# Optimization experiments

Hardware: AMD Instinct MI355X
Metric: run time of the kernel (lower is better)

## Reference

```python
import jax, jax.numpy as jnp
import numpy as np

H = 256
EPS = 1e-5
WIN = (-2, -1, 1, 2)  # radius_graph(pos/2^(d+1), k=2) on unit-spaced timestamps


def leaky(x):
    return jnp.where(x >= 0, x, 0.2 * x)


def layernorm(x, g, b):
    mu = jnp.mean(x, axis=-1, keepdims=True)
    var = jnp.mean(jnp.square(x - mu), axis=-1, keepdims=True)
    return (x - mu) * jax.lax.rsqrt(var + EPS) * g + b


def nbr_mean(x, offsets):
    # mean over temporal-window neighbors within each video row; [B,T,C]
    if not offsets:
        return jnp.zeros_like(x)
    T = x.shape[1]
    idx = jnp.arange(T)
    acc = jnp.zeros_like(x)
    cnt = jnp.zeros((T,), x.dtype)
    for o in offsets:
        valid = (idx + o >= 0) & (idx + o < T)
        acc = acc + jnp.where(valid[None, :, None], jnp.roll(x, -o, axis=1), 0.0)
        cnt = cnt + valid.astype(x.dtype)
    return acc / jnp.maximum(cnt, 1.0)[None, :, None]


def conv(x, Ws, Wn, b, offsets):
    # GraphConv with mean aggregation: W_self x_i + W_nbr mean_j x_j + b
    return x @ Ws + nbr_mean(x, offsets) @ Wn + b


def stage(x, s, Wself, Wnbr, bconv, ln_g, ln_b, offsets):
    # Dropout(eval)=id; conv; LeakyReLU(0.2); conv; LayerNorm; LeakyReLU(0.2)
    x = leaky(conv(x, Wself[s, 0], Wnbr[s, 0], bconv[s, 0], offsets))
    x = conv(x, Wself[s, 1], Wnbr[s, 1], bconv[s, 1], offsets)
    return leaky(layernorm(x, ln_g[s], ln_b[s]))


def upsample2(c):
    # knn_interpolate(k=2) from coarse (stride-2 subsampled) grid back to fine grid:
    # even fine nodes coincide with a coarse node (dist 0 -> weight ~inf -> copy);
    # odd fine nodes are equidistant from two coarse nodes (0.5/0.5), except the
    # last odd node whose 2-NN are at dist s and 3s -> weights 0.9/0.1.
    even = c
    nxt = jnp.concatenate([c[:, 1:], c[:, -1:]], axis=1)
    odd = 0.5 * (c + nxt)
    odd = odd.at[:, -1].set(0.9 * c[:, -1] + 0.1 * c[:, -2])
    B, Tc, C = c.shape
    return jnp.stack([even, odd], axis=2).reshape(B, 2 * Tc, C)


def setup_inputs() -> dict:
    key = jax.random.key(0)
    ks = jax.random.split(key, 8)
    B, T, F = 16, 4096, 1024
    N = B * T
    x = jax.random.normal(ks[0], (N, 1, F), dtype=jnp.float32)
    pos = (jnp.arange(N) % T).astype(jnp.float32)
    batch = (jnp.arange(N) // T).astype(jnp.int64)
    indices = (jnp.arange(N) % T).astype(jnp.int64)
    Wp = jax.random.normal(ks[1], (F, H), dtype=jnp.float32) / np.sqrt(F)
    bp = jnp.zeros((H,), jnp.float32)
    Wself = jax.random.normal(ks[2], (6, 2, H, H), dtype=jnp.float32) / np.sqrt(H)
    Wnbr = jax.random.normal(ks[3], (6, 2, H, H), dtype=jnp.float32) / np.sqrt(H)
    bconv = jnp.zeros((6, 2, H), jnp.float32)
    ln_g = jnp.ones((6, H), jnp.float32)
    ln_b = jnp.zeros((6, H), jnp.float32)
    return {"x": x, "pos": pos, "batch": batch, "indices": indices, "B": B, "T": T,
            "Wp": Wp, "bp": bp, "Wself": Wself, "Wnbr": Wnbr, "bconv": bconv,
            "ln_g": ln_g, "ln_b": ln_b}


def reference(x, pos, batch, indices, B, T, Wp, bp, Wself, Wnbr, bconv, ln_g, ln_b):
    # input projection: Rearrange 'B S F -> B (S F)' (S=1) + Linear
    feat = x.reshape(B, T, -1) @ Wp + bp  # [B,T,H]
    # ---- Temporal Encoder ----
    f = feat
    skips = [feat]  # depth-0 input graph features
    for d in range(3):
        f = f[:, ::2]  # batch_subsampling time pooling (stride 2)
        f = f + stage(f, d, Wself, Wnbr, bconv, ln_g, ln_b, WIN)
        if d < 2:
            skips.append(f)
    # ---- Function-Aware Decoder (eval path: clustering_at_inference=False) ----
    for i in range(3):
        res = skips[2 - i]
        f = res + upsample2(f)  # knn_interpolate(k=2) + skip
        dep = 2 - i
        # radius_graph(indices, 1.5): pooled index spacing 2^dep > 1.5 for dep>=1 -> no edges
        offs = WIN if dep == 0 else ()
        f = stage(f, 3 + i, Wself, Wnbr, bconv, ln_g, ln_b, offs)
    return f  # finest-resolution decoder output [B,T,H]
```

## Files before the change

### kernel.cpp

```cpp
#include <hip/hip_runtime.h>

#define HH 256

typedef __attribute__((ext_vector_type(8))) short short8;
typedef __attribute__((ext_vector_type(4))) float f32x4;
typedef __attribute__((ext_vector_type(4))) unsigned short u16x4;
typedef __attribute__((ext_vector_type(8))) unsigned short u16x8;

constexpr int NBATCH = 16;
constexpr int T0   = 4096;
constexpr int FDIM = 1024;
constexpr int R0   = NBATCH * T0;
constexpr int R1   = R0 / 2;
constexpr int R2   = R0 / 4;
constexpr int R3   = R0 / 8;

__device__ __forceinline__ float b2f(unsigned short u) {
    union { unsigned int i; float f; } v; v.i = ((unsigned int)u) << 16; return v.f;
}
__device__ __forceinline__ unsigned short f2b(float f) {
    union { float f; unsigned int i; } v; v.f = f;
    unsigned int r = v.i + 0x7fffu + ((v.i >> 16) & 1u);
    return (unsigned short)(r >> 16);
}
__device__ __forceinline__ void gload16(const void* g, void* l) {
    __builtin_amdgcn_global_load_lds((const __attribute__((address_space(1))) void*)g,
                                     (__attribute__((address_space(3))) void*)l, 16, 0, 0);
}
__device__ __forceinline__ void barrier_sync() {
    asm volatile("s_waitcnt lgkmcnt(0)\n\ts_barrier" ::: "memory");
}
__device__ __forceinline__ void wait_vm(int n) {
    switch (n) {
    case 2:  asm volatile("s_waitcnt vmcnt(2)"  ::: "memory"); break;
    case 3:  asm volatile("s_waitcnt vmcnt(3)"  ::: "memory"); break;
    case 4:  asm volatile("s_waitcnt vmcnt(4)"  ::: "memory"); break;
    case 5:  asm volatile("s_waitcnt vmcnt(5)"  ::: "memory"); break;
    case 6:  asm volatile("s_waitcnt vmcnt(6)"  ::: "memory"); break;
    default: asm volatile("s_waitcnt vmcnt(0)"  ::: "memory"); break;
    }
}
__device__ __forceinline__ int swz_ks(int chunk)        { return (chunk & 3) ^ ((chunk >> 3) & 3); }
__device__ __forceinline__ int frag_idx(int row, int g) { return (row * 4 + (g ^ ((row >> 1) & 3))) * 8; }

struct PVv { u16x8 v0, v1, v2, v3; };

__device__ __forceinline__ void transpose_tile(const float* __restrict__ src,
                                               unsigned short* __restrict__ dst,
                                               int K, int tilesPerMat, int bid, int tidx)
{
    int m = bid / tilesPerMat;
    int t = bid % tilesPerMat;
    int tr = t >> 3, tc = t & 7;
    const float* S = src + (size_t)m * K * HH;
    unsigned short* D = dst + (size_t)m * HH * K;
    __shared__ float tile[32][33];
    int x = tidx & 31, y = tidx >> 5;
#pragma unroll
    for (int i = y; i < 32; i += 8)
        tile[i][x] = S[(size_t)(tr * 32 + i) * HH + tc * 32 + x];
    __syncthreads();
#pragma unroll
    for (int i = y; i < 32; i += 8)
        D[(size_t)(tc * 32 + i) * K + tr * 32 + x] = f2b(tile[x][i]);
}

__global__ void transpose_all(const float* __restrict__ Wself, const float* __restrict__ Wnbr,
                              const float* __restrict__ Wp,
                              unsigned short* __restrict__ Ws_t, unsigned short* __restrict__ Wn_t,
                              unsigned short* __restrict__ Wp_t)
{
    int bid = blockIdx.x;
    if (bid < 768)       transpose_tile(Wself, Ws_t, HH,   64,  bid,        threadIdx.x);
    else if (bid < 1536) transpose_tile(Wnbr,  Wn_t, HH,   64,  bid - 768,  threadIdx.x);
    else                 transpose_tile(Wp,    Wp_t, FDIM, 256, bid - 1536, threadIdx.x);
}

template<int BM, int AMODE, int NBR, int LNFUSE, int OUT>
__launch_bounds__(512)
__global__ void conv_fused(const unsigned short* __restrict__ A,
                           const unsigned short* __restrict__ Cc,
                           const unsigned short* __restrict__ prev,
                           const unsigned short* __restrict__ Bself,
                           const unsigned short* __restrict__ Bnbr,
                           const float* __restrict__ bias,
                           const float* __restrict__ lng,
                           const float* __restrict__ lnb,
                           void* __restrict__ dstv,
                           int Tl, int Tc, int tlshift)
{
    constexpr int NT = NBR ? 16 : 8;
    constexpr int MF = (BM + 31) / 32;
    constexpr int WROWS = BM / 2;
    __shared__ unsigned short As[3][BM * 32];
    __shared__ unsigned short Bs[3][256 * 32];
    __shared__ float lnred[LNFUSE ? BM : 1][8];

    const int tid  = threadIdx.x;
    const int lane = tid & 63;
    const int w    = tid >> 6;
    const int wm   = w & 1, wn = w >> 1;
    const long row0 = (long)blockIdx.x * BM;

    const bool hasA   = (tid < BM * 4);
    const bool hasA_w = (w < (BM * 4) / 64);
    const int arr = tid >> 2;
    const int akk = swz_ks(tid);
    const long gr = row0 + (hasA ? arr : 0);

    float ca = 0.f, cb = 0.f; size_t rc0 = 0, rc1 = 0;
    if (AMODE == 2) {
        int t = (int)(gr & (long)(Tl - 1));
        long bq = gr >> tlshift;
        int k = t >> 1;
        rc0 = (size_t)bq * Tc + k;
        if (!(t & 1))        { ca = 1.0f; cb = 0.0f; rc1 = rc0; }
        else if (k < Tc - 1) { ca = 0.5f; cb = 0.5f; rc1 = rc0 + 1; }
        else                 { ca = 0.9f; cb = 0.1f; rc1 = rc0 - 1; }
    }
    float vinv = 1.f;
    float cf0 = 0.f, cf1 = 0.f, cf2 = 0.f, cf3 = 0.f;
    size_t nrow0 = 0, nrow1 = 0, nrow2 = 0, nrow3 = 0;
    if (NBR) {
        const int offs[4] = {-2, -1, 1, 2};
        int t = (int)(gr & (long)(Tl - 1));
        int cnt = 0;
        float cf[4]; size_t nr[4];
#pragma unroll
        for (int oi = 0; oi < 4; oi++) {
            int tn = t + offs[oi];
            bool v = (tn >= 0 && tn < Tl);
            cnt += v ? 1 : 0;
            int tcl = tn < 0 ? 0 : (tn > Tl - 1 ? Tl - 1 : tn);
            long r = gr - t + tcl;
            nr[oi] = (size_t)((AMODE == 1) ? 2 * r : r) * HH;
            cf[oi] = v ? 1.f : 0.f;
        }
        vinv = 1.f / (float)cnt;
        cf0 = cf[0]; cf1 = cf[1]; cf2 = cf[2]; cf3 = cf[3];
        nrow0 = nr[0]; nrow1 = nr[1]; nrow2 = nr[2]; nrow3 = nr[3];
    }

    f32x4 acc[MF][4] = {};
    PVv pvE = {}, pvO = {};

    auto Lof = [&](int t) -> int {
        if (!hasA_w) return 2;
        const int seg = (NBR && t >= 8) ? 1 : 0;
        return seg ? 6 : (AMODE == 2 ? 5 : 3);
    };
    auto issueB = [&](int t) {
        const int seg = (NBR && t >= 8) ? 1 : 0;
        const int k0 = (t & 7) * 32;
        const int sl = t % 3;
        const unsigned short* __restrict__ Bm = seg ? Bnbr : Bself;
        gload16(Bm + (size_t)arr * HH + k0 + akk * 8,         &Bs[sl][tid * 8]);
        gload16(Bm + (size_t)(128 + arr) * HH + k0 + akk * 8, &Bs[sl][(tid + 512) * 8]);
    };
    auto issueA = [&](int t, PVv& pv) {
        if (!hasA) return;
        const int seg = (NBR && t >= 8) ? 1 : 0;
        const int k0 = (t & 7) * 32;
        const int sl = t % 3;
        if (seg == 0) {
            if (AMODE == 0) {
                gload16(A + (size_t)gr * HH + k0 + akk * 8, &As[sl][tid * 8]);
            } else if (AMODE == 1) {
                gload16(A + (size_t)(2 * gr) * HH + k0 + akk * 8, &As[sl][tid * 8]);
            } else {
                pv.v0 = *(const u16x8*)(A + (size_t)gr * HH + k0 + akk * 8);
                pv.v1 = *(const u16x8*)(Cc + rc0 * HH + k0 + akk * 8);
                pv.v2 = *(const u16x8*)(Cc + rc1 * HH + k0 + akk * 8);
            }
        } else {
            pv.v0 = *(const u16x8*)(A + nrow0 + k0 + akk * 8);
            pv.v1 = *(const u16x8*)(A + nrow1 + k0 + akk * 8);
            pv.v2 = *(const u16x8*)(A + nrow2 + k0 + akk * 8);
            pv.v3 = *(const u16x8*)(A + nrow3 + k0 + akk * 8);
        }
    };
    auto finishA = [&](int t, PVv& pv) {
        if (!hasA) return;
        const int seg = (NBR && t >= 8) ? 1 : 0;
        const int sl = t % 3;
        if (seg == 0) {
            if (AMODE == 2) {
                u16x8 o;
#pragma unroll
                for (int j = 0; j < 8; j++)
                    o[j] = f2b(b2f(pv.v0[j]) + ca * b2f(pv.v1[j]) + cb * b2f(pv.v2[j]));
                *(u16x8*)&As[sl][tid * 8] = o;
            }
        } else {
            u16x8 o;
#pragma unroll
            for (int j = 0; j < 8; j++) {
                float a = cf0 * b2f(pv.v0[j]) + cf1 * b2f(pv.v1[j])
                        + cf2 * b2f(pv.v2[j]) + cf3 * b2f(pv.v3[j]);
                o[j] = f2b(a * vinv);
            }
            *(u16x8*)&As[sl][tid * 8] = o;
        }
    };

    issueB(0); issueA(0, pvE);
    issueB(1); issueA(1, pvO);
    wait_vm(Lof(1));
    finishA(0, pvE);
    barrier_sync();

#pragma unroll
    for (int t = 0; t < NT; ++t) {
        if (t + 2 < NT) {
            issueB(t + 2);
            if (((t + 2) & 1) == 0) issueA(t + 2, pvE); else issueA(t + 2, pvO);
        }

        const int sl = t % 3;
        __builtin_amdgcn_s_setprio(1);
        short8 af[MF], bg[4];
#pragma unroll
        for (int i = 0; i < MF; i++)
            af[i] = *(const short8*)&As[sl][frag_idx(wm * WROWS + i * 16 + (lane & 15), lane >> 4)];
#pragma unroll
        for (int i = 0; i < 4; i++)
            bg[i] = *(const short8*)&Bs[sl][frag_idx(wn * 64 + i * 16 + (lane & 15), lane >> 4)];
#pragma unroll
        for (int mi = 0; mi < MF; mi++)
#pragma unroll
            for (int ni = 0; ni < 4; ni++)
                acc[mi][ni] = __builtin_amdgcn_mfma_f32_16x16x32_bf16(af[mi], bg[ni], acc[mi][ni], 0, 0, 0);
        __builtin_amdgcn_s_setprio(0);

        if (t + 1 < NT) {
            wait_vm((t + 2 < NT) ? Lof(t + 2) : 0);
            if (((t + 1) & 1) == 0) finishA(t + 1, pvE); else finishA(t + 1, pvO);
            barrier_sync();
        }
    }

    if (LNFUSE == 0) {
        unsigned short* outp = (unsigned short*)dstv;
#pragma unroll
        for (int mi = 0; mi < MF; mi++) {
            size_t rbase = (size_t)row0 + wm * WROWS + mi * 16 + (lane >> 4) * 4;
#pragma unroll
            for (int ni = 0; ni < 4; ni++) {
                int c = wn * 64 + ni * 16 + (lane & 15);
                float bb = bias[c];
                f32x4 v = acc[mi][ni];
#pragma unroll
                for (int r = 0; r < 4; r++) {
                    float t = v[r] + bb;
                    t = (t >= 0.f) ? t : 0.2f * t;
                    outp[(rbase + r) * HH + c] = f2b(t);
                }
            }
        }
    } else {
        float bb[4];
#pragma unroll
        for (int ni = 0; ni < 4; ni++) bb[ni] = bias[wn * 64 + ni * 16 + (lane & 15)];

#pragma unroll
        for (int mi = 0; mi < MF; mi++) {
#pragma unroll
            for (int r = 0; r < 4; r++) {
                float s = 0.f, q = 0.f;
#pragma unroll
                for (int ni = 0; ni < 4; ni++) {
                    float v = acc[mi][ni][r] + bb[ni];
                    s += v; q += v * v;
                }
                s += __shfl_xor(s, 1); q += __shfl_xor(q, 1);
                s += __shfl_xor(s, 2); q += __shfl_xor(q, 2);
                s += __shfl_xor(s, 4); q += __shfl_xor(q, 4);
                s += __shfl_xor(s, 8); q += __shfl_xor(q, 8);
                if ((lane & 15) == 0) {
                    int row = wm * WROWS + mi * 16 + (lane >> 4) * 4 + r;
                    lnred[row][wn]     = s;
                    lnred[row][4 + wn] = q;
                }
            }
        }
        __syncthreads();

        float gv[4], bv[4];
#pragma unroll
        for (int ni = 0; ni < 4; ni++) {
            int c = wn * 64 + ni * 16 + (lane & 15);
            gv[ni] = lng[c]; bv[ni] = lnb[c];
        }

#pragma unroll
        for (int mi = 0; mi < MF; mi++) {
#pragma unroll
            for (int r = 0; r < 4; r++) {
                int row = wm * WROWS + mi * 16 + (lane >> 4) * 4 + r;
                float s = lnred[row][0] + lnred[row][1] + lnred[row][2] + lnred[row][3];
                float q = lnred[row][4] + lnred[row][5] + lnred[row][6] + lnred[row][7];
                float mu  = s * (1.0f / HH);
                float var = q * (1.0f / HH) - mu * mu;
                float inv = rsqrtf(var + 1e-5f);
                size_t grow = (size_t)row0 + row;
#pragma unroll
                for (int ni = 0; ni < 4; ni++) {
                    int c = wn * 64 + ni * 16 + (lane & 15);
                    float v = acc[mi][ni][r] + bb[ni];
                    float y = (v - mu) * inv * gv[ni] + bv[ni];
                    y = (y >= 0.f) ? y : 0.2f * y;
                    if (OUT == 2) {
                        ((float*)dstv)[grow * HH + c] = y;
                    } else {
                        if (OUT == 1) y += b2f(prev[(2 * grow) * HH + c]);
                        ((unsigned short*)dstv)[grow * HH + c] = f2b(y);
                    }
                }
            }
        }
    }
}

__launch_bounds__(512)
__global__ void proj_gemm(const float* __restrict__ A, const unsigned short* __restrict__ Bt,
                          const float* __restrict__ bias, unsigned short* __restrict__ out)
{
    constexpr int NT = FDIM / 32;
    __shared__ unsigned short As[3][128 * 32];
    __shared__ unsigned short Bs[3][256 * 32];
    const int tid  = threadIdx.x;
    const int lane = tid & 63;
    const int w    = tid >> 6;
    const int wm   = w & 1, wn = w >> 1;
    const size_t row0 = (size_t)blockIdx.x * 128;

    const int arr = tid >> 2;
    const int akk = swz_ks(tid);

    f32x4 acc[4][4] = {};
    float4 paE0, paE1, paO0, paO1;

    auto issue = [&](int t, float4& p0, float4& p1) {
        const int k0 = t * 32;
        const int sl = t % 3;
        gload16(Bt + (size_t)arr * FDIM + k0 + akk * 8,         &Bs[sl][tid * 8]);
        gload16(Bt + (size_t)(128 + arr) * FDIM + k0 + akk * 8, &Bs[sl][(tid + 512) * 8]);
        const float* s = A + (row0 + arr) * (size_t)FDIM + k0 + akk * 8;
        p0 = *(const float4*)s;
        p1 = *(const float4*)(s + 4);
    };
    auto finish = [&](int t, float4& p0, float4& p1) {
        const int sl = t % 3;
        u16x8 o = { f2b(p0.x), f2b(p0.y), f2b(p0.z), f2b(p0.w),
                    f2b(p1.x), f2b(p1.y), f2b(p1.z), f2b(p1.w) };
        *(u16x8*)&As[sl][tid * 8] = o;
    };

    issue(0, paE0, paE1);
    issue(1, paO0, paO1);
    wait_vm(4);
    finish(0, paE0, paE1);
    barrier_sync();

#pragma unroll
    for (int t = 0; t < NT; ++t) {
        if (t + 2 < NT) {
            if (((t + 2) & 1) == 0) issue(t + 2, paE0, paE1); else issue(t + 2, paO0, paO1);
        }

        const int sl = t % 3;
        __builtin_amdgcn_s_setprio(1);
        short8 af[4], bg[4];
#pragma unroll
        for (int i = 0; i < 4; i++) {
            af[i] = *(const short8*)&As[sl][frag_idx(wm * 64 + i * 16 + (lane & 15), lane >> 4)];
            bg[i] = *(const short8*)&Bs[sl][frag_idx(wn * 64 + i * 16 + (lane & 15), lane >> 4)];
        }
#pragma unroll
        for (int mi = 0; mi < 4; mi++)
#pragma unroll
            for (int ni = 0; ni < 4; ni++)
                acc[mi][ni] = __builtin_amdgcn_mfma_f32_16x16x32_bf16(af[mi], bg[ni], acc[mi][ni], 0, 0, 0);
        __builtin_amdgcn_s_setprio(0);

        if (t + 1 < NT) {
            wait_vm((t + 2 < NT) ? 4 : 0);
            if (((t + 1) & 1) == 0) finish(t + 1, paE0, paE1); else finish(t + 1, paO0, paO1);
            barrier_sync();
        }
    }

#pragma unroll
    for (int mi = 0; mi < 4; mi++) {
        size_t rbase = row0 + wm * 64 + mi * 16 + (lane >> 4) * 4;
#pragma unroll
        for (int ni = 0; ni < 4; ni++) {
            int c = wn * 64 + ni * 16 + (lane & 15);
            float bb = bias[c];
            f32x4 v = acc[mi][ni];
#pragma unroll
            for (int r = 0; r < 4; r++)
                out[(rbase + r) * HH + c] = f2b(v[r] + bb);
        }
    }
}

__global__ void upsample_add_kernel(unsigned short* __restrict__ res, const unsigned short* __restrict__ c,
                                    int Tc, int tlshift, int Rout)
{
    int idx = blockIdx.x * 256 + threadIdx.x;
    int r = idx >> 5, cc = (idx & 31) * 8;
    if (r >= Rout) return;
    int Tl = Tc * 2;
    int t  = r & (Tl - 1);
    int bq = r >> tlshift;
    int k  = t >> 1;
    size_t rc = (size_t)bq * Tc + k;
    float u[8];
    if (!(t & 1)) {
        u16x8 v = *(const u16x8*)(c + rc * HH + cc);
#pragma unroll
        for (int j = 0; j < 8; j++) u[j] = b2f(v[j]);
    } else if (k < Tc - 1) {
        u16x8 v0 = *(const u16x8*)(c + rc * HH + cc);
        u16x8 v1 = *(const u16x8*)(c + (rc + 1) * HH + cc);
#pragma unroll
        for (int j = 0; j < 8; j++) u[j] = 0.5f * (b2f(v0[j]) + b2f(v1[j]));
    } else {
        u16x8 v0 = *(const u16x8*)(c + rc * HH + cc);
        u16x8 vm = *(const u16x8*)(c + (rc - 1) * HH + cc);
#pragma unroll
        for (int j = 0; j < 8; j++) u[j] = 0.9f * b2f(v0[j]) + 0.1f * b2f(vm[j]);
    }
    u16x8 rv = *(const u16x8*)(res + (size_t)r * HH + cc);
    u16x8 o;
#pragma unroll
    for (int j = 0; j < 8; j++) o[j] = f2b(b2f(rv[j]) + u[j]);
    *(u16x8*)(res + (size_t)r * HH + cc) = o;
}

extern "C" void kernel_launch(void* const* d_in, const int* in_sizes, int n_in,
                              void* d_out, int out_size, void* d_ws, size_t ws_size,
                              hipStream_t stream)
{
    const float* x     = (const float*)d_in[0];
    const float* Wp    = (const float*)d_in[6];
    const float* bp    = (const float*)d_in[7];
    const float* Wself = (const float*)d_in[8];
    const float* Wnbr  = (const float*)d_in[9];
    const float* bconv = (const float*)d_in[10];
    const float* ln_g  = (const float*)d_in[11];
    const float* ln_b  = (const float*)d_in[12];
    float* out = (float*)d_out;

    char* p = (char*)d_ws;
    unsigned short* Wself_t = (unsigned short*)p; p += (size_t)12 * HH * HH * 2;
    unsigned short* Wnbr_t  = (unsigned short*)p; p += (size_t)12 * HH * HH * 2;
    unsigned short* Wp_t    = (unsigned short*)p; p += (size_t)HH * FDIM * 2;
    unsigned short* c0 = (unsigned short*)p; p += (size_t)R0 * HH * 2;
    unsigned short* c1 = (unsigned short*)p; p += (size_t)R1 * HH * 2;
    unsigned short* c2 = (unsigned short*)p; p += (size_t)R2 * HH * 2;
    unsigned short* c3 = (unsigned short*)p; p += (size_t)R3 * HH * 2;
    unsigned short* t1 = (unsigned short*)p; p += (size_t)R0 * HH * 2;
    if (ws_size < (size_t)(p - (char*)d_ws)) return;

    auto Ws = [&](int i) { return Wself_t + (size_t)i * HH * HH; };
    auto Wn = [&](int i) { return Wnbr_t  + (size_t)i * HH * HH; };

    transpose_all<<<1792, 256, 0, stream>>>(Wself, Wnbr, Wp, Wself_t, Wnbr_t, Wp_t);

    proj_gemm<<<R0 / 128, 512, 0, stream>>>(x, Wp_t, bp, c0);

    conv_fused<128, 1, 1, 0, 0><<<R1 / 128, 512, 0, stream>>>(c0, nullptr, nullptr, Ws(0), Wn(0),
        bconv + 0 * HH, nullptr, nullptr, t1, 2048, 0, 0);
    conv_fused<128, 0, 1, 1, 1><<<R1 / 128, 512, 0, stream>>>(t1, nullptr, c0, Ws(1), Wn(1),
        bconv + 1 * HH, ln_g + 0 * HH, ln_b + 0 * HH, c1, 2048, 0, 0);

    conv_fused<64, 1, 1, 0, 0><<<R2 / 64, 512, 0, stream>>>(c1, nullptr, nullptr, Ws(2), Wn(2),
        bconv + 2 * HH, nullptr, nullptr, t1, 1024, 0, 0);
    conv_fused<64, 0, 1, 1, 1><<<R2 / 64, 512, 0, stream>>>(t1, nullptr, c1, Ws(3), Wn(3),
        bconv + 3 * HH, ln_g + 1 * HH, ln_b + 1 * HH, c2, 1024, 0, 0);

    conv_fused<32, 1, 1, 0, 0><<<R3 / 32, 512, 0, stream>>>(c2, nullptr, nullptr, Ws(4), Wn(4),
        bconv + 4 * HH, nullptr, nullptr, t1, 512, 0, 0);
    conv_fused<32, 0, 1, 1, 1><<<R3 / 32, 512, 0, stream>>>(t1, nullptr, c2, Ws(5), Wn(5),
        bconv + 5 * HH, ln_g + 2 * HH, ln_b + 2 * HH, c3, 512, 0, 0);

    conv_fused<64, 2, 0, 0, 0><<<R2 / 64, 512, 0, stream>>>(c2, c3, nullptr, Ws(6), nullptr,
        bconv + 6 * HH, nullptr, nullptr, t1, 1024, 512, 10);
    conv_fused<64, 0, 0, 1, 0><<<R2 / 64, 512, 0, stream>>>(t1, nullptr, nullptr, Ws(7), nullptr,
        bconv + 7 * HH, ln_g + 3 * HH, ln_b + 3 * HH, c2, 1024, 0, 0);

    conv_fused<128, 2, 0, 0, 0><<<R1 / 128, 512, 0, stream>>>(c1, c2, nullptr, Ws(8), nullptr,
        bconv + 8 * HH, nullptr, nullptr, t1, 2048, 1024, 11);
    conv_fused<128, 0, 0, 1, 0><<<R1 / 128, 512, 0, stream>>>(t1, nullptr, nullptr, Ws(9), nullptr,
        bconv + 9 * HH, ln_g + 4 * HH, ln_b + 4 * HH, c1, 2048, 0, 0);

    upsample_add_kernel<<<R0 / 8, 256, 0, stream>>>(c0, c1, 2048, 12, R0);
    conv_fused<128, 0, 1, 0, 0><<<R0 / 128, 512, 0, stream>>>(c0, nullptr, nullptr, Ws(10), Wn(10),
        bconv + 10 * HH, nullptr, nullptr, t1, 4096, 0, 0);
    conv_fused<128, 0, 1, 1, 2><<<R0 / 128, 512, 0, stream>>>(t1, nullptr, nullptr, Ws(11), Wn(11),
        bconv + 11 * HH, ln_g + 5 * HH, ln_b + 5 * HH, out, 4096, 0, 0);
}
```

Measured before the change: 353.1 us.

## Single-buffer register-staged A loads and raise occupancy via launch bounds

Replaces the even/odd double set of register-staged A-tile prefetch buffers with a single buffer. The register-path load for tile t+2 is now issued after tile t+1 is finished into shared memory, and the vmcnt wait counts shrink to match. Both GEMM kernels also declare launch_bounds(512,4) to cap registers and allow more resident waves. The cost is a shorter prefetch distance for register-staged loads, which exposes more global latency, and possible spills under the tighter register cap.

Result: slower. 411.4 us (+16.5%).

```diff
diff --git a/kernel.cpp b/kernel.cpp
--- a/kernel.cpp
+++ b/kernel.cpp
@@ -77,7 +77,7 @@
 }
 
 template<int BM, int AMODE, int NBR, int LNFUSE, int OUT>
-__launch_bounds__(512)
+__launch_bounds__(512, 4)
 __global__ void conv_fused(const unsigned short* __restrict__ A,
                            const unsigned short* __restrict__ Cc,
                            const unsigned short* __restrict__ prev,
@@ -142,32 +142,33 @@
     }
 
     f32x4 acc[MF][4] = {};
-    PVv pvE = {}, pvO = {};
-
-    auto Lof = [&](int t) -> int {
+    PVv pv = {};
+
+    auto NG = [&](int t) -> int {
         if (!hasA_w) return 2;
         const int seg = (NBR && t >= 8) ? 1 : 0;
-        return seg ? 6 : (AMODE == 2 ? 5 : 3);
-    };
-    auto issueB = [&](int t) {
+        return (seg == 0 && AMODE <= 1) ? 3 : 2;
+    };
+    auto issueG = [&](int t) {
         const int seg = (NBR && t >= 8) ? 1 : 0;
         const int k0 = (t & 7) * 32;
         const int sl = t % 3;
         const unsigned short* __restrict__ Bm = seg ? Bnbr : Bself;
         gload16(Bm + (size_t)arr * HH + k0 + akk * 8,         &Bs[sl][tid * 8]);
         gload16(Bm + (size_t)(128 + arr) * HH + k0 + akk * 8, &Bs[sl][(tid + 512) * 8]);
-    };
-    auto issueA = [&](int t, PVv& pv) {
+        if (hasA && seg == 0 && AMODE <= 1) {
+            if (AMODE == 0)
+                gload16(A + (size_t)gr * HH + k0 + akk * 8, &As[sl][tid * 8]);
+            else
+                gload16(A + (size_t)(2 * gr) * HH + k0 + akk * 8, &As[sl][tid * 8]);
+        }
+    };
+    auto issueR = [&](int t) {
         if (!hasA) return;
         const int seg = (NBR && t >= 8) ? 1 : 0;
         const int k0 = (t & 7) * 32;
-        const int sl = t % 3;
         if (seg == 0) {
-            if (AMODE == 0) {
-                gload16(A + (size_t)gr * HH + k0 + akk * 8, &As[sl][tid * 8]);
-            } else if (AMODE == 1) {
-                gload16(A + (size_t)(2 * gr) * HH + k0 + akk * 8, &As[sl][tid * 8]);
-            } else {
+            if (AMODE == 2) {
                 pv.v0 = *(const u16x8*)(A + (size_t)gr * HH + k0 + akk * 8);
                 pv.v1 = *(const u16x8*)(Cc + rc0 * HH + k0 + akk * 8);
                 pv.v2 = *(const u16x8*)(Cc + rc1 * HH + k0 + akk * 8);
@@ -179,7 +180,7 @@
             pv.v3 = *(const u16x8*)(A + nrow3 + k0 + akk * 8);
         }
     };
-    auto finishA = [&](int t, PVv& pv) {
+    auto finishA = [&](int t) {
         if (!hasA) return;
         const int seg = (NBR && t >= 8) ? 1 : 0;
         const int sl = t % 3;
@@ -203,18 +204,17 @@
         }
     };
 
-    issueB(0); issueA(0, pvE);
-    issueB(1); issueA(1, pvO);
-    wait_vm(Lof(1));
-    finishA(0, pvE);
+    issueG(0);
+    issueR(0);
+    issueG(1);
+    wait_vm(NG(1));
+    finishA(0);
+    issueR(1);
     barrier_sync();
 
 #pragma unroll
     for (int t = 0; t < NT; ++t) {
-        if (t + 2 < NT) {
-            issueB(t + 2);
-            if (((t + 2) & 1) == 0) issueA(t + 2, pvE); else issueA(t + 2, pvO);
-        }
+        if (t + 2 < NT) issueG(t + 2);
 
         const int sl = t % 3;
         __builtin_amdgcn_s_setprio(1);
@@ -233,8 +233,9 @@
         __builtin_amdgcn_s_setprio(0);
 
         if (t + 1 < NT) {
-            wait_vm((t + 2 < NT) ? Lof(t + 2) : 0);
-            if (((t + 1) & 1) == 0) finishA(t + 1, pvE); else finishA(t + 1, pvO);
+            wait_vm((t + 2 < NT) ? NG(t + 2) : 0);
+            finishA(t + 1);
+            if (t + 2 < NT) issueR(t + 2);
             barrier_sync();
         }
     }
@@ -321,7 +322,7 @@
     }
 }
 
-__launch_bounds__(512)
+__launch_bounds__(512, 4)
 __global__ void proj_gemm(const float* __restrict__ A, const unsigned short* __restrict__ Bt,
                           const float* __restrict__ bias, unsigned short* __restrict__ out)
 {
@@ -338,35 +339,38 @@
     const int akk = swz_ks(tid);
 
     f32x4 acc[4][4] = {};
-    float4 paE0, paE1, paO0, paO1;
-
-    auto issue = [&](int t, float4& p0, float4& p1) {
+    float4 pa0, pa1;
+
+    auto issueG = [&](int t) {
         const int k0 = t * 32;
         const int sl = t % 3;
         gload16(Bt + (size_t)arr * FDIM + k0 + akk * 8,         &Bs[sl][tid * 8]);
         gload16(Bt + (size_t)(128 + arr) * FDIM + k0 + akk * 8, &Bs[sl][(tid + 512) * 8]);
+    };
+    auto issueR = [&](int t) {
+        const int k0 = t * 32;
         const float* s = A + (row0 + arr) * (size_t)FDIM + k0 + akk * 8;
-        p0 = *(const float4*)s;
-        p1 = *(const float4*)(s + 4);
-    };
-    auto finish = [&](int t, float4& p0, float4& p1) {
+        pa0 = *(const float4*)s;
+        pa1 = *(const float4*)(s + 4);
+    };
+    auto finish = [&](int t) {
         const int sl = t % 3;
-        u16x8 o = { f2b(p0.x), f2b(p0.y), f2b(p0.z), f2b(p0.w),
-                    f2b(p1.x), f2b(p1.y), f2b(p1.z), f2b(p1.w) };
+        u16x8 o = { f2b(pa0.x), f2b(pa0.y), f2b(pa0.z), f2b(pa0.w),
+                    f2b(pa1.x), f2b(pa1.y), f2b(pa1.z), f2b(pa1.w) };
         *(u16x8*)&As[sl][tid * 8] = o;
     };
 
-    issue(0, paE0, paE1);
-    issue(1, paO0, paO1);
-    wait_vm(4);
-    finish(0, paE0, paE1);
+    issueG(0);
+    issueR(0);
+    issueG(1);
+    wait_vm(2);
+    finish(0);
+    issueR(1);
     barrier_sync();
 
 #pragma unroll
     for (int t = 0; t < NT; ++t) {
-        if (t + 2 < NT) {
-            if (((t + 2) & 1) == 0) issue(t + 2, paE0, paE1); else issue(t + 2, paO0, paO1);
-        }
+        if (t + 2 < NT) issueG(t + 2);
 
         const int sl = t % 3;
         __builtin_amdgcn_s_setprio(1);
@@ -384,8 +388,9 @@
         __builtin_amdgcn_s_setprio(0);
 
         if (t + 1 < NT) {
-            wait_vm((t + 2 < NT) ? 4 : 0);
-            if (((t + 1) & 1) == 0) finish(t + 1, paE0, paE1); else finish(t + 1, paO0, paO1);
+            wait_vm((t + 2 < NT) ? 2 : 0);
+            finish(t + 1);
+            if (t + 2 < NT) issueR(t + 2);
             barrier_sync();
         }
     }
```

## Fuse both decoder-stage convs into one kernel keeping intermediate in LDS

Applied to the files above, without the earlier changes.

Adds up_stage_fused, which performs the upsample+skip add, the first self-only conv with LeakyReLU, stores the intermediate activations in shared memory, then runs the second conv with LayerNorm and LeakyReLU in the same kernel. This replaces two kernel launches per decoder stage for depths 2 and 1, and removes the global write and re-read of the intermediate tensor. The cost is a larger LDS footprint (an extra BM×256 bf16 buffer), which may reduce occupancy. The depth-1 stage also moves from 128-row to 64-row tiles. The output is written in place over the skip input, which appears safe because each block reads only its own rows of that buffer.

After: 350.1 us (median of 2 runs). About the same (-0.8%).

```diff
diff --git a/kernel.cpp b/kernel.cpp
--- a/kernel.cpp
+++ b/kernel.cpp
@@ -42,6 +42,7 @@
 }
 __device__ __forceinline__ int swz_ks(int chunk)        { return (chunk & 3) ^ ((chunk >> 3) & 3); }
 __device__ __forceinline__ int frag_idx(int row, int g) { return (row * 4 + (g ^ ((row >> 1) & 3))) * 8; }
+__device__ __forceinline__ int a2_idx(int row, int g)   { return (row * 32 + (g ^ (row & 31))) * 8; }
 
 struct PVv { u16x8 v0, v1, v2, v3; };
 
@@ -321,6 +322,231 @@
     }
 }
 
+template<int BM>
+__launch_bounds__(512)
+__global__ void up_stage_fused(const unsigned short* __restrict__ A,
+                               const unsigned short* __restrict__ Cc,
+                               const unsigned short* __restrict__ B1,
+                               const float* __restrict__ b1,
+                               const unsigned short* __restrict__ B2,
+                               const float* __restrict__ b2,
+                               const float* __restrict__ lng,
+                               const float* __restrict__ lnb,
+                               unsigned short* __restrict__ dst,
+                               int Tl, int Tc, int tlshift)
+{
+    constexpr int MF = BM / 32;
+    constexpr int WROWS = BM / 2;
+    __shared__ unsigned short As[3][BM * 32];
+    __shared__ unsigned short Bs[3][256 * 32];
+    __shared__ unsigned short A2[BM * 256];
+    __shared__ float lnred[BM][8];
+
+    const int tid  = threadIdx.x;
+    const int lane = tid & 63;
+    const int w    = tid >> 6;
+    const int wm   = w & 1, wn = w >> 1;
+    const long row0 = (long)blockIdx.x * BM;
+
+    const bool hasA   = (tid < BM * 4);
+    const bool hasA_w = (w < (BM * 4) / 64);
+    const int arr = tid >> 2;
+    const int akk = swz_ks(tid);
+    const long gr = row0 + (hasA ? arr : 0);
+
+    float ca, cb; size_t rc0, rc1;
+    {
+        int t = (int)(gr & (long)(Tl - 1));
+        long bq = gr >> tlshift;
+        int k = t >> 1;
+        rc0 = (size_t)bq * Tc + k;
+        if (!(t & 1))        { ca = 1.0f; cb = 0.0f; rc1 = rc0; }
+        else if (k < Tc - 1) { ca = 0.5f; cb = 0.5f; rc1 = rc0 + 1; }
+        else                 { ca = 0.9f; cb = 0.1f; rc1 = rc0 - 1; }
+    }
+
+    f32x4 acc[MF][4] = {};
+    PVv pvE = {}, pvO = {};
+
+    auto issueB1 = [&](int t) {
+        const int k0 = t * 32;
+        const int sl = t % 3;
+        gload16(B1 + (size_t)arr * HH + k0 + akk * 8,         &Bs[sl][tid * 8]);
+        gload16(B1 + (size_t)(128 + arr) * HH + k0 + akk * 8, &Bs[sl][(tid + 512) * 8]);
+    };
+    auto issueA1 = [&](int t, PVv& pv) {
+        if (!hasA) return;
+        const int k0 = t * 32;
+        pv.v0 = *(const u16x8*)(A + (size_t)gr * HH + k0 + akk * 8);
+        pv.v1 = *(const u16x8*)(Cc + rc0 * HH + k0 + akk * 8);
+        pv.v2 = *(const u16x8*)(Cc + rc1 * HH + k0 + akk * 8);
+    };
+    auto finishA1 = [&](int t, PVv& pv) {
+        if (!hasA) return;
+        const int sl = t % 3;
+        u16x8 o;
+#pragma unroll
+        for (int j = 0; j < 8; j++)
+            o[j] = f2b(b2f(pv.v0[j]) + ca * b2f(pv.v1[j]) + cb * b2f(pv.v2[j]));
+        *(u16x8*)&As[sl][tid * 8] = o;
+    };
+    const int L1 = hasA_w ? 5 : 2;
+
+    issueB1(0); issueA1(0, pvE);
+    issueB1(1); issueA1(1, pvO);
+    wait_vm(L1);
+    finishA1(0, pvE);
+    barrier_sync();
+
+#pragma unroll
+    for (int t = 0; t < 8; ++t) {
+        if (t + 2 < 8) {
+            issueB1(t + 2);
+            if (((t + 2) & 1) == 0) issueA1(t + 2, pvE); else issueA1(t + 2, pvO);
+        }
+        const int sl = t % 3;
+        __builtin_amdgcn_s_setprio(1);
+        short8 af[MF], bg[4];
+#pragma unroll
+        for (int i = 0; i < MF; i++)
+            af[i] = *(const short8*)&As[sl][frag_idx(wm * WROWS + i * 16 + (lane & 15), lane >> 4)];
+#pragma unroll
+        for (int i = 0; i < 4; i++)
+            bg[i] = *(const short8*)&Bs[sl][frag_idx(wn * 64 + i * 16 + (lane & 15), lane >> 4)];
+#pragma unroll
+        for (int mi = 0; mi < MF; mi++)
+#pragma unroll
+            for (int ni = 0; ni < 4; ni++)
+                acc[mi][ni] = __builtin_amdgcn_mfma_f32_16x16x32_bf16(af[mi], bg[ni], acc[mi][ni], 0, 0, 0);
+        __builtin_amdgcn_s_setprio(0);
+        if (t + 1 < 8) {
+            wait_vm((t + 2 < 8) ? L1 : 0);
+            if (((t + 1) & 1) == 0) finishA1(t + 1, pvE); else finishA1(t + 1, pvO);
+            barrier_sync();
+        }
+    }
+
+#pragma unroll
+    for (int mi = 0; mi < MF; mi++) {
+#pragma unroll
+        for (int ni = 0; ni < 4; ni++) {
+            int c = wn * 64 + ni * 16 + (lane & 15);
+            float bb1 = b1[c];
+            int g = c >> 3, e = c & 7;
+            f32x4 v = acc[mi][ni];
+#pragma unroll
+            for (int r = 0; r < 4; r++) {
+                int row = wm * WROWS + mi * 16 + (lane >> 4) * 4 + r;
+                float t = v[r] + bb1;
+                t = (t >= 0.f) ? t : 0.2f * t;
+                A2[a2_idx(row, g) + e] = f2b(t);
+            }
+        }
+    }
+    __syncthreads();
+
+#pragma unroll
+    for (int mi = 0; mi < MF; mi++)
+#pragma unroll
+        for (int ni = 0; ni < 4; ni++)
+            acc[mi][ni] = f32x4{};
+
+    auto issueB2 = [&](int t) {
+        const int k0 = t * 32;
+        const int sl = t % 3;
+        gload16(B2 + (size_t)arr * HH + k0 + akk * 8,         &Bs[sl][tid * 8]);
+        gload16(B2 + (size_t)(128 + arr) * HH + k0 + akk * 8, &Bs[sl][(tid + 512) * 8]);
+    };
+
+    issueB2(0);
+    issueB2(1);
+    wait_vm(2);
+    barrier_sync();
+
+#pragma unroll
+    for (int t = 0; t < 8; ++t) {
+        if (t + 2 < 8) issueB2(t + 2);
+        const int sl = t % 3;
+        __builtin_amdgcn_s_setprio(1);
+        short8 af[MF], bg[4];
+#pragma unroll
+        for (int i = 0; i < MF; i++) {
+            int row = wm * WROWS + i * 16 + (lane & 15);
+            int g = t * 4 + (lane >> 4);
+            af[i] = *(const short8*)&A2[a2_idx(row, g)];
+        }
+#pragma unroll
+        for (int i = 0; i < 4; i++)
+            bg[i] = *(const short8*)&Bs[sl][frag_idx(wn * 64 + i * 16 + (lane & 15), lane >> 4)];
+#pragma unroll
+        for (int mi = 0; mi < MF; mi++)
+#pragma unroll
+            for (int ni = 0; ni < 4; ni++)
+                acc[mi][ni] = __builtin_amdgcn_mfma_f32_16x16x32_bf16(af[mi], bg[ni], acc[mi][ni], 0, 0, 0);
+        __builtin_amdgcn_s_setprio(0);
+        if (t + 1 < 8) {
+            wait_vm((t + 2 < 8) ? 2 : 0);
+            barrier_sync();
+        }
+    }
+
+    float bb[4];
+#pragma unroll
+    for (int ni = 0; ni < 4; ni++) bb[ni] = b2[wn * 64 + ni * 16 + (lane & 15)];
+
+#pragma unroll
+    for (int mi = 0; mi < MF; mi++) {
+#pragma unroll
+        for (int r = 0; r < 4; r++) {
+            float s = 0.f, q = 0.f;
+#pragma unroll
+            for (int ni = 0; ni < 4; ni++) {
+                float v = acc[mi][ni][r] + bb[ni];
+                s += v; q += v * v;
+            }
+            s += __shfl_xor(s, 1); q += __shfl_xor(q, 1);
+            s += __shfl_xor(s, 2); q += __shfl_xor(q, 2);
+            s += __shfl_xor(s, 4); q += __shfl_xor(q, 4);
+            s += __shfl_xor(s, 8); q += __shfl_xor(q, 8);
+            if ((lane & 15) == 0) {
+                int row = wm * WROWS + mi * 16 + (lane >> 4) * 4 + r;
+                lnred[row][wn]     = s;
+                lnred[row][4 + wn] = q;
+            }
+        }
+    }
+    __syncthreads();
+
+    float gv[4], bv[4];
+#pragma unroll
+    for (int ni = 0; ni < 4; ni++) {
+        int c = wn * 64 + ni * 16 + (lane & 15);
+        gv[ni] = lng[c]; bv[ni] = lnb[c];
+    }
+
+#pragma unroll
+    for (int mi = 0; mi < MF; mi++) {
+#pragma unroll
+        for (int r = 0; r < 4; r++) {
+            int row = wm * WROWS + mi * 16 + (lane >> 4) * 4 + r;
+            float s = lnred[row][0] + lnred[row][1] + lnred[row][2] + lnred[row][3];
+            float q = lnred[row][4] + lnred[row][5] + lnred[row][6] + lnred[row][7];
+            float mu  = s * (1.0f / HH);
+            float var = q * (1.0f / HH) - mu * mu;
+            float inv = rsqrtf(var + 1e-5f);
+            size_t grow = (size_t)row0 + row;
+#pragma unroll
+            for (int ni = 0; ni < 4; ni++) {
+                int c = wn * 64 + ni * 16 + (lane & 15);
+                float v = acc[mi][ni][r] + bb[ni];
+                float y = (v - mu) * inv * gv[ni] + bv[ni];
+                y = (y >= 0.f) ? y : 0.2f * y;
+                dst[grow * HH + c] = f2b(y);
+            }
+        }
+    }
+}
+
 __launch_bounds__(512)
 __global__ void proj_gemm(const float* __restrict__ A, const unsigned short* __restrict__ Bt,
                           const float* __restrict__ bias, unsigned short* __restrict__ out)
@@ -486,15 +712,11 @@
     conv_fused<32, 0, 1, 1, 1><<<R3 / 32, 512, 0, stream>>>(t1, nullptr, c2, Ws(5), Wn(5),
         bconv + 5 * HH, ln_g + 2 * HH, ln_b + 2 * HH, c3, 512, 0, 0);
 
-    conv_fused<64, 2, 0, 0, 0><<<R2 / 64, 512, 0, stream>>>(c2, c3, nullptr, Ws(6), nullptr,
-        bconv + 6 * HH, nullptr, nullptr, t1, 1024, 512, 10);
-    conv_fused<64, 0, 0, 1, 0><<<R2 / 64, 512, 0, stream>>>(t1, nullptr, nullptr, Ws(7), nullptr,
-        bconv + 7 * HH, ln_g + 3 * HH, ln_b + 3 * HH, c2, 1024, 0, 0);
-
-    conv_fused<128, 2, 0, 0, 0><<<R1 / 128, 512, 0, stream>>>(c1, c2, nullptr, Ws(8), nullptr,
-        bconv + 8 * HH, nullptr, nullptr, t1, 2048, 1024, 11);
-    conv_fused<128, 0, 0, 1, 0><<<R1 / 128, 512, 0, stream>>>(t1, nullptr, nullptr, Ws(9), nullptr,
-        bconv + 9 * HH, ln_g + 4 * HH, ln_b + 4 * HH, c1, 2048, 0, 0);
+    up_stage_fused<64><<<R2 / 64, 512, 0, stream>>>(c2, c3, Ws(6), bconv + 6 * HH,
+        Ws(7), bconv + 7 * HH, ln_g + 3 * HH, ln_b + 3 * HH, c2, 1024, 512, 10);
+
+    up_stage_fused<64><<<R1 / 64, 512, 0, stream>>>(c1, c2, Ws(8), bconv + 8 * HH,
+        Ws(9), bconv + 9 * HH, ln_g + 4 * HH, ln_b + 4 * HH, c1, 2048, 1024, 11);
 
     upsample_add_kernel<<<R0 / 8, 256, 0, stream>>>(c0, c1, 2048, 12, R0);
     conv_fused<128, 0, 1, 0, 0><<<R0 / 128, 512, 0, stream>>>(c0, nullptr, nullptr, Ws(10), Wn(10),
```
